# Kernel optimization log

Hardware: AMD Instinct MI355X
Metric: run time of the kernel (lower is better)

## Reference

```python
import jax, jax.numpy as jnp
import numpy as np

H = 16  # n_heads


def setup_inputs() -> dict:
    key = jax.random.key(0)
    ks = jax.random.split(key, 11)
    B, S, D = 2, 2048, 1024
    def rn(k, shape, scale=1.0):
        return jax.random.normal(k, shape, dtype=jnp.float32) * scale
    w_scale = 1.0 / np.sqrt(D)
    return {
        "queries": rn(ks[0], (B, S, D)),
        "keys": rn(ks[1], (B, S, D)),
        "values": rn(ks[2], (B, S, D)),
        "Wq": rn(ks[3], (D, D), w_scale), "bq": rn(ks[4], (D,), 0.02),
        "Wk": rn(ks[5], (D, D), w_scale), "bk": rn(ks[6], (D,), 0.02),
        "Wv": rn(ks[7], (D, D), w_scale), "bv": rn(ks[8], (D,), 0.02),
        "Wo": rn(ks[9], (D, D), w_scale), "bo": rn(ks[10], (D,), 0.02),
    }


def _split_heads(x, h):
    # [B, S, D] -> [B, h, S, D/h]
    B, S, D = x.shape
    return x.reshape(B, S, h, D // h).transpose(0, 2, 1, 3)


def reference(queries, keys, values, Wq, bq, Wk, bk, Wv, bv, Wo, bo):
    B, S, D = queries.shape
    Q = _split_heads(queries @ Wq + bq, H)  # [B,h,S,dk]
    K = _split_heads(keys @ Wk + bk, H)
    V = _split_heads(values @ Wv + bv, H)
    # Faithful quirk: scale by sqrt(seq_len), not sqrt(d_k)
    factor = jnp.sqrt(jnp.asarray(S, dtype=Q.dtype))
    scores = jnp.einsum("bhqd,bhkd->bhqk", Q, K) / factor  # [B,h,S,S]
    weights = jax.nn.softmax(scores, axis=-1)
    attn = jnp.einsum("bhqk,bhkd->bhqd", weights, V)  # [B,h,S,dk]
    attn = attn.transpose(0, 2, 1, 3).reshape(B, S, D)  # [B,S,D]
    return attn @ Wo + bo
```

## Files before the change

kernel.cpp:

```cpp
#include <hip/hip_runtime.h>

typedef unsigned short ushort_t;
typedef unsigned int uint_t;
typedef __attribute__((ext_vector_type(8))) short short8;
typedef __attribute__((ext_vector_type(4))) float floatx4;

#define QSCALE 0.03187936f

__device__ __forceinline__ ushort_t f2bf(float f) {
    union { float f; uint_t u; } c; c.f = f;
    uint_t u = c.u;
    return (ushort_t)((u + 0x7fffu + ((u >> 16) & 1u)) >> 16);
}
__device__ __forceinline__ floatx4 mfma16x32(short8 a, short8 b, floatx4 c) {
    return __builtin_amdgcn_mfma_f32_16x16x32_bf16(a, b, c, 0, 0, 0);
}
__device__ __forceinline__ floatx4 zero4() { floatx4 z = {0.f, 0.f, 0.f, 0.f}; return z; }

__device__ __forceinline__ void gload16(const ushort_t* g, ushort_t* l) {
    __builtin_amdgcn_global_load_lds(
        (const __attribute__((address_space(1))) void*)g,
        (__attribute__((address_space(3))) void*)l, 16, 0, 0);
}

__global__ __launch_bounds__(256) void cvt_bf16(
    const float* __restrict__ s0, const float* __restrict__ s1,
    const float* __restrict__ s2, ushort_t* __restrict__ d0,
    ushort_t* __restrict__ d1, ushort_t* __restrict__ d2)
{
    const int which = blockIdx.x >> 11;
    const int blk = blockIdx.x & 2047;
    const float* src = (which == 0) ? s0 : (which == 1) ? s1 : s2;
    ushort_t* dst = (which == 0) ? d0 : (which == 1) ? d1 : d2;
    const int i = (blk * 256 + threadIdx.x) * 8;
    float4 f0 = *(const float4*)(src + i);
    float4 f1 = *(const float4*)(src + i + 4);
    __align__(16) ushort_t t[8];
    t[0] = f2bf(f0.x); t[1] = f2bf(f0.y); t[2] = f2bf(f0.z); t[3] = f2bf(f0.w);
    t[4] = f2bf(f1.x); t[5] = f2bf(f1.y); t[6] = f2bf(f1.z); t[7] = f2bf(f1.w);
    *(uint4*)(dst + i) = *(uint4*)t;
}

__global__ __launch_bounds__(256) void transpose_w(
    const float* __restrict__ W0, const float* __restrict__ W1,
    const float* __restrict__ W2, const float* __restrict__ W3,
    ushort_t* __restrict__ WT)
{
    __shared__ ushort_t tile[64][65];
    const float* W = (blockIdx.y == 0) ? W0 : (blockIdx.y == 1) ? W1
                   : (blockIdx.y == 2) ? W2 : W3;
    ushort_t* dst = WT + (size_t)blockIdx.y * (1024 * 1024);
    const int t = threadIdx.x;
    const int r = t >> 2, p = t & 3;
    const int j0 = (blockIdx.x & 15) << 6, k0 = (blockIdx.x >> 4) << 6;

    const float* src = W + (size_t)(k0 + r) * 1024 + j0 + p * 16;
    float4 f0 = *(const float4*)(src);
    float4 f1 = *(const float4*)(src + 4);
    float4 f2 = *(const float4*)(src + 8);
    float4 f3 = *(const float4*)(src + 12);
    ushort_t* tr = &tile[r][p * 16];
    tr[0] = f2bf(f0.x); tr[1] = f2bf(f0.y); tr[2]  = f2bf(f0.z); tr[3]  = f2bf(f0.w);
    tr[4] = f2bf(f1.x); tr[5] = f2bf(f1.y); tr[6]  = f2bf(f1.z); tr[7]  = f2bf(f1.w);
    tr[8] = f2bf(f2.x); tr[9] = f2bf(f2.y); tr[10] = f2bf(f2.z); tr[11] = f2bf(f2.w);
    tr[12] = f2bf(f3.x); tr[13] = f2bf(f3.y); tr[14] = f2bf(f3.z); tr[15] = f2bf(f3.w);
    __syncthreads();
    __align__(16) ushort_t buf[16];
#pragma unroll
    for (int i = 0; i < 16; ++i) buf[i] = tile[p * 16 + i][r];
    ushort_t* o = dst + (size_t)(j0 + r) * 1024 + k0 + p * 16;
    *(uint4*)(o)     = *(uint4*)(buf);
    *(uint4*)(o + 8) = *(uint4*)(buf + 8);
}

__global__ __launch_bounds__(256) void gemm_bt(
    const ushort_t* __restrict__ A0, const ushort_t* __restrict__ A1,
    const ushort_t* __restrict__ A2, const ushort_t* __restrict__ WT,
    const float* __restrict__ b0, const float* __restrict__ b1,
    const float* __restrict__ b2,
    ushort_t* __restrict__ Dq, ushort_t* __restrict__ Dk,
    ushort_t* __restrict__ Dv, int zbase)
{
    __shared__ __align__(16) ushort_t As[128 * 32];
    __shared__ __align__(16) ushort_t Bs[128 * 32];

    const int mode = blockIdx.z + zbase;
    const ushort_t* A = (mode == 0) ? A0 : (mode == 1) ? A1 : A2;
    const float* bias = (mode == 0) ? b0 : (mode == 1) ? b1 : b2;
    const ushort_t* Bt = WT + (size_t)mode * 1048576;

    const int tid = threadIdx.x;
    const int lane = tid & 63, wid = tid >> 6;
    const int quad = lane >> 4, l16 = lane & 15;
    const int wm = wid >> 1, wn = wid & 1;
    const int row0 = blockIdx.y << 7, col0 = blockIdx.x << 7;

    floatx4 acc[4][4];
#pragma unroll
    for (int i = 0; i < 4; ++i)
#pragma unroll
        for (int j = 0; j < 4; ++j) acc[i][j] = zero4();

    const int i0 = tid, i1 = 256 + tid;
    const int r0_ = i0 >> 2, c0_ = (i0 & 3) ^ (r0_ & 3);
    const int r1_ = i1 >> 2, c1_ = (i1 & 3) ^ (r1_ & 3);
    const ushort_t* gA0 = A  + (size_t)(row0 + r0_) * 1024 + c0_ * 8;
    const ushort_t* gA1 = A  + (size_t)(row0 + r1_) * 1024 + c1_ * 8;
    const ushort_t* gB0 = Bt + (size_t)(col0 + r0_) * 1024 + c0_ * 8;
    const ushort_t* gB1 = Bt + (size_t)(col0 + r1_) * 1024 + c1_ * 8;
    ushort_t* lA0 = As + i0 * 8;  ushort_t* lA1 = As + i1 * 8;
    ushort_t* lB0 = Bs + i0 * 8;  ushort_t* lB1 = Bs + i1 * 8;

    const int ra = wm * 64 + l16, rb = wn * 64 + l16;
    const int sa_off = (quad ^ (l16 & 3)) * 8;

    for (int k0 = 0; k0 < 1024; k0 += 32) {
        __syncthreads();
        gload16(gA0 + k0, lA0);
        gload16(gA1 + k0, lA1);
        gload16(gB0 + k0, lB0);
        gload16(gB1 + k0, lB1);
        __syncthreads();

        short8 af[4], bf[4];
#pragma unroll
        for (int i = 0; i < 4; ++i)
            af[i] = *(const short8*)(As + (ra + i * 16) * 32 + sa_off);
#pragma unroll
        for (int j = 0; j < 4; ++j)
            bf[j] = *(const short8*)(Bs + (rb + j * 16) * 32 + sa_off);
#pragma unroll
        for (int i = 0; i < 4; ++i)
#pragma unroll
            for (int j = 0; j < 4; ++j)
                acc[i][j] = mfma16x32(af[i], bf[j], acc[i][j]);
    }

    const float sc = (mode == 0) ? QSCALE : 1.f;
#pragma unroll
    for (int i = 0; i < 4; ++i) {
#pragma unroll
        for (int j = 0; j < 4; ++j) {
            const int c = col0 + wn * 64 + j * 16 + l16;
            const float bv = bias[c];
#pragma unroll
            for (int rr = 0; rr < 4; ++rr) {
                const int r = row0 + wm * 64 + i * 16 + quad * 4 + rr;
                const float v = (acc[i][j][rr] + bv) * sc;
                const int b = r >> 11, s = r & 2047, h = c >> 6, d = c & 63;
                if (mode <= 1) {
                    ushort_t* D = (mode == 0) ? Dq : Dk;
                    D[(((b * 16 + h) * 2048 + s) << 6) + d] = f2bf(v);
                } else {
                    Dv[(((b * 16 + h) * 64 + d) << 11) + s] = f2bf(v);
                }
            }
        }
    }
}

__global__ __launch_bounds__(256) void gemm64(
    const ushort_t* __restrict__ A, const ushort_t* __restrict__ Bt,
    const float* __restrict__ bias, float* __restrict__ Dout)
{
    __shared__ __align__(16) ushort_t As[64 * 32];
    __shared__ __align__(16) ushort_t Bs[128 * 32];
    const int tid = threadIdx.x;
    const int lane = tid & 63, wid = tid >> 6;
    const int quad = lane >> 4, l16 = lane & 15;
    const int wm = wid >> 1, wn = wid & 1;
    const int row0 = blockIdx.y << 6, col0 = blockIdx.x << 7;

    floatx4 acc[2][4];
#pragma unroll
    for (int i = 0; i < 2; ++i)
#pragma unroll
        for (int j = 0; j < 4; ++j) acc[i][j] = zero4();

    const int rA = tid >> 2, cA = (tid & 3) ^ (rA & 3);
    const ushort_t* gA = A + (size_t)(row0 + rA) * 1024 + cA * 8;
    ushort_t* lA = As + tid * 8;
    const int i0 = tid, i1 = 256 + tid;
    const int rB0 = i0 >> 2, cB0 = (i0 & 3) ^ (rB0 & 3);
    const int rB1 = i1 >> 2, cB1 = (i1 & 3) ^ (rB1 & 3);
    const ushort_t* gB0 = Bt + (size_t)(col0 + rB0) * 1024 + cB0 * 8;
    const ushort_t* gB1 = Bt + (size_t)(col0 + rB1) * 1024 + cB1 * 8;
    ushort_t* lB0 = Bs + i0 * 8;  ushort_t* lB1 = Bs + i1 * 8;

    const int sa_off = (quad ^ (l16 & 3)) * 8;

    for (int k0 = 0; k0 < 1024; k0 += 32) {
        __syncthreads();
        gload16(gA + k0, lA);
        gload16(gB0 + k0, lB0);
        gload16(gB1 + k0, lB1);
        __syncthreads();

        short8 af[2], bf[4];
#pragma unroll
        for (int i = 0; i < 2; ++i)
            af[i] = *(const short8*)(As + (wm * 32 + i * 16 + l16) * 32 + sa_off);
#pragma unroll
        for (int j = 0; j < 4; ++j)
            bf[j] = *(const short8*)(Bs + (wn * 64 + j * 16 + l16) * 32 + sa_off);
#pragma unroll
        for (int i = 0; i < 2; ++i)
#pragma unroll
            for (int j = 0; j < 4; ++j)
                acc[i][j] = mfma16x32(af[i], bf[j], acc[i][j]);
    }

#pragma unroll
    for (int i = 0; i < 2; ++i)
#pragma unroll
        for (int j = 0; j < 4; ++j) {
            const int c = col0 + wn * 64 + j * 16 + l16;
            const float bv = bias[c];
#pragma unroll
            for (int rr = 0; rr < 4; ++rr) {
                const int r = row0 + wm * 32 + i * 16 + quad * 4 + rr;
                Dout[(size_t)r * 1024 + c] = acc[i][j][rr] + bv;
            }
        }
}

__global__ __launch_bounds__(256, 2) void attn64q(
    const ushort_t* __restrict__ Q, const ushort_t* __restrict__ K,
    const ushort_t* __restrict__ Vt, ushort_t* __restrict__ Out)
{
    __shared__ __align__(16) ushort_t Ks[2][2][64 * 64];
    __shared__ __align__(16) ushort_t Vs[2][2][64 * 64];

    const int tid = threadIdx.x;
    const int lane = tid & 63, wid = tid >> 6;
    const int quad = lane >> 4, l16 = lane & 15;
    const int blk = blockIdx.x;
    const int bh = blk & 31;
    const int q0 = (blk >> 5) << 7;

    const ushort_t* Qh = Q + (size_t)bh * (2048 * 64);
    const ushort_t* Kh = K + (size_t)bh * (2048 * 64);
    const ushort_t* Vh = Vt + (size_t)bh * (64 * 2048);

    short8 qf0[2], qf1[2];
#pragma unroll
    for (int u = 0; u < 2; ++u) {
        const int qr = q0 + wid * 32 + u * 16 + l16;
        qf0[u] = *(const short8*)(Qh + (size_t)qr * 64 + quad * 8);
        qf1[u] = *(const short8*)(Qh + (size_t)qr * 64 + 32 + quad * 8);
    }

    floatx4 o_acc[2][4], lsum[2];
#pragma unroll
    for (int u = 0; u < 2; ++u) {
        lsum[u] = zero4();
#pragma unroll
        for (int d = 0; d < 4; ++d) o_acc[u][d] = zero4();
    }

    const int kr = tid >> 3, kc = (tid & 7) ^ (kr & 7);
    const ushort_t* gK0 = Kh + (size_t)kr * 64 + kc * 8;
    const ushort_t* gV0 = Vh + (size_t)kr * 2048 + kc * 8;

    const int l7 = l16 & 7;
    const int q2 = quad >> 1, q1 = (quad & 1) * 4;

    union { uint_t u4[4]; short8 s; } onep;
    onep.u4[0] = onep.u4[1] = onep.u4[2] = onep.u4[3] = 0x3f803f80u;
    const short8 ones = onep.s;

#define STAGE(pp, kto) do {                                                  \
        _Pragma("unroll")                                                    \
        for (int hf_ = 0; hf_ < 2; ++hf_) {                                  \
            gload16(gK0 + (size_t)(kto) * 64 + hf_ * 4096,                   \
                    &Ks[pp][hf_][tid * 8]);                                  \
            gload16(gK0 + (size_t)(kto) * 64 + hf_ * 4096 + 2048,            \
                    &Ks[pp][hf_][tid * 8 + 2048]);                           \
            gload16(gV0 + (kto) + hf_ * 64,                                  \
                    &Vs[pp][hf_][tid * 8]);                                  \
            gload16(gV0 + (kto) + hf_ * 64 + 65536,                          \
                    &Vs[pp][hf_][tid * 8 + 2048]);                           \
        }                                                                    \
    } while (0)

    STAGE(0, 0);
    for (int it = 0; it < 16; ++it) {
        const int p = it & 1;
        __syncthreads();
        if (it < 15) STAGE(p ^ 1, (it + 1) * 128);

#pragma unroll
        for (int hf = 0; hf < 2; ++hf) {
            const ushort_t* ksp = &Ks[p][hf][0];
            const ushort_t* vsp = &Vs[p][hf][0];

            floatx4 sa[2][4];
#pragma unroll
            for (int g = 0; g < 4; ++g) {
                const int row = g * 16 + l16;
                const short8 kf0 = *(const short8*)(ksp + row * 64 + ((quad ^ l7) * 8));
                const short8 kf1 = *(const short8*)(ksp + row * 64 + (((quad + 4) ^ l7) * 8));
#pragma unroll
                for (int u = 0; u < 2; ++u) {
                    floatx4 t0 = mfma16x32(kf0, qf0[u], zero4());
                    sa[u][g] = mfma16x32(kf1, qf1[u], t0);
                }
            }

#pragma unroll
            for (int G = 0; G < 2; ++G) {
                short8 pf[2];
#pragma unroll
                for (int u = 0; u < 2; ++u) {
                    uint_t ub[8];
#pragma unroll
                    for (int t = 0; t < 8; ++t) {
                        const int g = G * 2 + (t >> 2), r = t & 3;
                        const float e = __builtin_amdgcn_exp2f(fminf(sa[u][g][r], 80.f));
                        ub[t] = __float_as_uint(e);
                    }
                    union { uint_t u4[4]; short8 s; } pc;
                    pc.u4[0] = __builtin_amdgcn_perm(ub[1], ub[0], 0x07060302u);
                    pc.u4[1] = __builtin_amdgcn_perm(ub[3], ub[2], 0x07060302u);
                    pc.u4[2] = __builtin_amdgcn_perm(ub[5], ub[4], 0x07060302u);
                    pc.u4[3] = __builtin_amdgcn_perm(ub[7], ub[6], 0x07060302u);
                    pf[u] = pc.s;
                    lsum[u] = mfma16x32(pf[u], ones, lsum[u]);
                }
                const int ch0 = ((4 * G + q2) ^ l7) * 8;
                const int ch1 = ((4 * G + 2 + q2) ^ l7) * 8;
#pragma unroll
                for (int db = 0; db < 4; ++db) {
                    const int vbase = (db * 16 + l16) * 64 + q1;
                    const uint2 v0 = *(const uint2*)(vsp + vbase + ch0);
                    const uint2 v1 = *(const uint2*)(vsp + vbase + ch1);
                    union { uint_t u4[4]; short8 s; } vc;
                    vc.u4[0] = v0.x; vc.u4[1] = v0.y; vc.u4[2] = v1.x; vc.u4[3] = v1.y;
                    o_acc[0][db] = mfma16x32(pf[0], vc.s, o_acc[0][db]);
                    o_acc[1][db] = mfma16x32(pf[1], vc.s, o_acc[1][db]);
                }
            }
        }
    }
#undef STAGE

    const int b = bh >> 4, hh = bh & 15;
#pragma unroll
    for (int u = 0; u < 2; ++u) {
        const int s0 = q0 + wid * 32 + u * 16 + quad * 4;
#pragma unroll
        for (int r = 0; r < 4; ++r) {
            const float inv = 1.f / lsum[u][r];
#pragma unroll
            for (int db = 0; db < 4; ++db) {
                const float v = o_acc[u][db][r] * inv;
                Out[(size_t)(b * 2048 + s0 + r) * 1024 + hh * 64 + db * 16 + l16] = f2bf(v);
            }
        }
    }
}

extern "C" void kernel_launch(void* const* d_in, const int* in_sizes, int n_in,
                              void* d_out, int out_size, void* d_ws, size_t ws_size,
                              hipStream_t stream) {
    const float* queries = (const float*)d_in[0];
    const float* keys    = (const float*)d_in[1];
    const float* values  = (const float*)d_in[2];
    const float* Wq = (const float*)d_in[3];
    const float* bq = (const float*)d_in[4];
    const float* Wk = (const float*)d_in[5];
    const float* bk = (const float*)d_in[6];
    const float* Wv = (const float*)d_in[7];
    const float* bv = (const float*)d_in[8];
    const float* Wo = (const float*)d_in[9];
    const float* bo = (const float*)d_in[10];
    float* out = (float*)d_out;

    char* ws = (char*)d_ws;
    const size_t MB = 1024 * 1024;
    ushort_t* WT = (ushort_t*)(ws);
    const ushort_t* WoT = WT + 3 * 1048576;
    dim3 tb(256);

    transpose_w<<<dim3(256, 4), tb, 0, stream>>>(Wq, Wk, Wv, Wo, WT);

    if (ws_size >= 64 * MB) {
        ushort_t* Qb  = (ushort_t*)(ws + 8 * MB);
        ushort_t* Kb  = (ushort_t*)(ws + 16 * MB);
        ushort_t* Vb  = (ushort_t*)(ws + 24 * MB);
        ushort_t* Qp  = (ushort_t*)(ws + 32 * MB);
        ushort_t* Kp  = (ushort_t*)(ws + 40 * MB);
        ushort_t* Vtp = (ushort_t*)(ws + 48 * MB);
        ushort_t* An  = (ushort_t*)(ws + 56 * MB);
        cvt_bf16<<<dim3(6144), tb, 0, stream>>>(queries, keys, values, Qb, Kb, Vb);
        gemm_bt<<<dim3(8, 32, 3), tb, 0, stream>>>(Qb, Kb, Vb, WT,
            bq, bk, bv, Qp, Kp, Vtp, 0);
        attn64q<<<dim3(512), tb, 0, stream>>>(Qp, Kp, Vtp, An);
        gemm64<<<dim3(8, 64), tb, 0, stream>>>(An, WoT, bo, out);
    } else {
        ushort_t* buf1 = (ushort_t*)(ws + 8 * MB);
        ushort_t* buf2 = (ushort_t*)(ws + 16 * MB);
        ushort_t* Qp   = (ushort_t*)(ws + 24 * MB);
        ushort_t* Kp   = (ushort_t*)(ws + 32 * MB);
        cvt_bf16<<<dim3(4096), tb, 0, stream>>>(queries, keys, keys, buf1, buf2, buf2);
        gemm_bt<<<dim3(8, 32, 2), tb, 0, stream>>>(buf1, buf2, buf2, WT,
            bq, bk, bk, Qp, Kp, Kp, 0);
        cvt_bf16<<<dim3(2048), tb, 0, stream>>>(values, values, values, buf1, buf1, buf1);
        gemm_bt<<<dim3(8, 32, 1), tb, 0, stream>>>(buf1, buf1, buf1, WT,
            bv, bv, bv, buf2, buf2, buf2, 2);
        attn64q<<<dim3(512), tb, 0, stream>>>(Qp, Kp, buf2, buf1);
        gemm64<<<dim3(8, 64), tb, 0, stream>>>(buf1, WoT, bo, out);
    }
}
```

Baseline: 229.6 us.

## Split attention block across 8 waves with 16 query rows each

The attention kernel now launches 512 threads per block, so each of the eight waves owns 16 query rows instead of 32. Each thread issues half as many K/V tile loads into LDS, and per-thread accumulator and score register use is halved. The goal is more waves in flight to hide latency and better balance the MFMA and exp work. In exchange each K/V fragment read from LDS feeds only one MFMA instead of two, which doubles LDS read traffic per unit of compute, and the larger blocks may limit how many fit on a CU.

```diff
diff --git a/kernel.cpp b/kernel.cpp
--- a/kernel.cpp
+++ b/kernel.cpp
@@ -224,7 +224,7 @@
         }
 }
 
-__global__ __launch_bounds__(256, 2) void attn64q(
+__global__ __launch_bounds__(512, 2) void attn64q(
     const ushort_t* __restrict__ Q, const ushort_t* __restrict__ K,
     const ushort_t* __restrict__ Vt, ushort_t* __restrict__ Out)
 {
@@ -242,21 +242,13 @@
     const ushort_t* Kh = K + (size_t)bh * (2048 * 64);
     const ushort_t* Vh = Vt + (size_t)bh * (64 * 2048);
 
-    short8 qf0[2], qf1[2];
-#pragma unroll
-    for (int u = 0; u < 2; ++u) {
-        const int qr = q0 + wid * 32 + u * 16 + l16;
-        qf0[u] = *(const short8*)(Qh + (size_t)qr * 64 + quad * 8);
-        qf1[u] = *(const short8*)(Qh + (size_t)qr * 64 + 32 + quad * 8);
-    }
-
-    floatx4 o_acc[2][4], lsum[2];
-#pragma unroll
-    for (int u = 0; u < 2; ++u) {
-        lsum[u] = zero4();
-#pragma unroll
-        for (int d = 0; d < 4; ++d) o_acc[u][d] = zero4();
-    }
+    const int qr = q0 + wid * 16 + l16;
+    const short8 qf0 = *(const short8*)(Qh + (size_t)qr * 64 + quad * 8);
+    const short8 qf1 = *(const short8*)(Qh + (size_t)qr * 64 + 32 + quad * 8);
+
+    floatx4 o_acc[4], lsum = zero4();
+#pragma unroll
+    for (int d = 0; d < 4; ++d) o_acc[d] = zero4();
 
     const int kr = tid >> 3, kc = (tid & 7) ^ (kr & 7);
     const ushort_t* gK0 = Kh + (size_t)kr * 64 + kc * 8;
@@ -274,12 +266,8 @@
         for (int hf_ = 0; hf_ < 2; ++hf_) {                                  \
             gload16(gK0 + (size_t)(kto) * 64 + hf_ * 4096,                   \
                     &Ks[pp][hf_][tid * 8]);                                  \
-            gload16(gK0 + (size_t)(kto) * 64 + hf_ * 4096 + 2048,            \
-                    &Ks[pp][hf_][tid * 8 + 2048]);                           \
             gload16(gV0 + (kto) + hf_ * 64,                                  \
                     &Vs[pp][hf_][tid * 8]);                                  \
-            gload16(gV0 + (kto) + hf_ * 64 + 65536,                          \
-                    &Vs[pp][hf_][tid * 8 + 2048]);                           \
         }                                                                    \
     } while (0)
 
@@ -294,39 +282,33 @@
             const ushort_t* ksp = &Ks[p][hf][0];
             const ushort_t* vsp = &Vs[p][hf][0];
 
-            floatx4 sa[2][4];
+            floatx4 sa[4];
 #pragma unroll
             for (int g = 0; g < 4; ++g) {
                 const int row = g * 16 + l16;
                 const short8 kf0 = *(const short8*)(ksp + row * 64 + ((quad ^ l7) * 8));
                 const short8 kf1 = *(const short8*)(ksp + row * 64 + (((quad + 4) ^ l7) * 8));
-#pragma unroll
-                for (int u = 0; u < 2; ++u) {
-                    floatx4 t0 = mfma16x32(kf0, qf0[u], zero4());
-                    sa[u][g] = mfma16x32(kf1, qf1[u], t0);
+                floatx4 t0 = mfma16x32(kf0, qf0, zero4());
+                sa[g] = mfma16x32(kf1, qf1, t0);
+            }
+
+#pragma unroll
+            for (int G = 0; G < 2; ++G) {
+                uint_t ub[8];
+#pragma unroll
+                for (int t = 0; t < 8; ++t) {
+                    const int g = G * 2 + (t >> 2), r = t & 3;
+                    const float e = __builtin_amdgcn_exp2f(fminf(sa[g][r], 80.f));
+                    ub[t] = __float_as_uint(e);
                 }
-            }
-
-#pragma unroll
-            for (int G = 0; G < 2; ++G) {
-                short8 pf[2];
-#pragma unroll
-                for (int u = 0; u < 2; ++u) {
-                    uint_t ub[8];
-#pragma unroll
-                    for (int t = 0; t < 8; ++t) {
-                        const int g = G * 2 + (t >> 2), r = t & 3;
-                        const float e = __builtin_amdgcn_exp2f(fminf(sa[u][g][r], 80.f));
-                        ub[t] = __float_as_uint(e);
-                    }
-                    union { uint_t u4[4]; short8 s; } pc;
-                    pc.u4[0] = __builtin_amdgcn_perm(ub[1], ub[0], 0x07060302u);
-                    pc.u4[1] = __builtin_amdgcn_perm(ub[3], ub[2], 0x07060302u);
-                    pc.u4[2] = __builtin_amdgcn_perm(ub[5], ub[4], 0x07060302u);
-                    pc.u4[3] = __builtin_amdgcn_perm(ub[7], ub[6], 0x07060302u);
-                    pf[u] = pc.s;
-                    lsum[u] = mfma16x32(pf[u], ones, lsum[u]);
-                }
+                union { uint_t u4[4]; short8 s; } pc;
+                pc.u4[0] = __builtin_amdgcn_perm(ub[1], ub[0], 0x07060302u);
+                pc.u4[1] = __builtin_amdgcn_perm(ub[3], ub[2], 0x07060302u);
+                pc.u4[2] = __builtin_amdgcn_perm(ub[5], ub[4], 0x07060302u);
+                pc.u4[3] = __builtin_amdgcn_perm(ub[7], ub[6], 0x07060302u);
+                const short8 pf = pc.s;
+                lsum = mfma16x32(pf, ones, lsum);
+
                 const int ch0 = ((4 * G + q2) ^ l7) * 8;
                 const int ch1 = ((4 * G + 2 + q2) ^ l7) * 8;
 #pragma unroll
@@ -336,8 +318,7 @@
                     const uint2 v1 = *(const uint2*)(vsp + vbase + ch1);
                     union { uint_t u4[4]; short8 s; } vc;
                     vc.u4[0] = v0.x; vc.u4[1] = v0.y; vc.u4[2] = v1.x; vc.u4[3] = v1.y;
-                    o_acc[0][db] = mfma16x32(pf[0], vc.s, o_acc[0][db]);
-                    o_acc[1][db] = mfma16x32(pf[1], vc.s, o_acc[1][db]);
+                    o_acc[db] = mfma16x32(pf, vc.s, o_acc[db]);
                 }
             }
         }
@@ -345,17 +326,14 @@
 #undef STAGE
 
     const int b = bh >> 4, hh = bh & 15;
-#pragma unroll
-    for (int u = 0; u < 2; ++u) {
-        const int s0 = q0 + wid * 32 + u * 16 + quad * 4;
-#pragma unroll
-        for (int r = 0; r < 4; ++r) {
-            const float inv = 1.f / lsum[u][r];
-#pragma unroll
-            for (int db = 0; db < 4; ++db) {
-                const float v = o_acc[u][db][r] * inv;
-                Out[(size_t)(b * 2048 + s0 + r) * 1024 + hh * 64 + db * 16 + l16] = f2bf(v);
-            }
+    const int s0 = q0 + wid * 16 + quad * 4;
+#pragma unroll
+    for (int r = 0; r < 4; ++r) {
+        const float inv = 1.f / lsum[r];
+#pragma unroll
+        for (int db = 0; db < 4; ++db) {
+            const float v = o_acc[db][r] * inv;
+            Out[(size_t)(b * 2048 + s0 + r) * 1024 + hh * 64 + db * 16 + l16] = f2bf(v);
         }
     }
 }
@@ -381,6 +359,7 @@
     ushort_t* WT = (ushort_t*)(ws);
     const ushort_t* WoT = WT + 3 * 1048576;
     dim3 tb(256);
+    dim3 ta(512);
 
     transpose_w<<<dim3(256, 4), tb, 0, stream>>>(Wq, Wk, Wv, Wo, WT);
 
@@ -395,7 +374,7 @@
         cvt_bf16<<<dim3(6144), tb, 0, stream>>>(queries, keys, values, Qb, Kb, Vb);
         gemm_bt<<<dim3(8, 32, 3), tb, 0, stream>>>(Qb, Kb, Vb, WT,
             bq, bk, bv, Qp, Kp, Vtp, 0);
-        attn64q<<<dim3(512), tb, 0, stream>>>(Qp, Kp, Vtp, An);
+        attn64q<<<dim3(512), ta, 0, stream>>>(Qp, Kp, Vtp, An);
         gemm64<<<dim3(8, 64), tb, 0, stream>>>(An, WoT, bo, out);
     } else {
         ushort_t* buf1 = (ushort_t*)(ws + 8 * MB);
@@ -408,7 +387,7 @@
         cvt_bf16<<<dim3(2048), tb, 0, stream>>>(values, values, values, buf1, buf1, buf1);
         gemm_bt<<<dim3(8, 32, 1), tb, 0, stream>>>(buf1, buf1, buf1, WT,
             bv, bv, bv, buf2, buf2, buf2, 2);
-        attn64q<<<dim3(512), tb, 0, stream>>>(Qp, Kp, buf2, buf1);
+        attn64q<<<dim3(512), ta, 0, stream>>>(Qp, Kp, buf2, buf1);
         gemm64<<<dim3(8, 64), tb, 0, stream>>>(buf1, WoT, bo, out);
     }
 }
```

Result: no change. 228.9 us (-0.3%).

## Fuse weight transpose into input conversion and remap GEMM blocks across XCDs

Applied to the files above, without the earlier changes.

Merges the bf16 conversion of inputs and the weight transpose/convert into one `prep` kernel, removing a separate launch. Both GEMM kernels now use a flat 1-D grid with a swizzled block index, so consecutive tiles sharing A/B panels land on the same XCD and its L2 cache. The transposed V projection epilogue now writes four consecutive sequence elements as one 8-byte store instead of four scalar stores. Costs are extra index arithmetic, and the fallback path now converts `keys` twice inside `prep`.

```diff
diff --git a/kernel.cpp b/kernel.cpp
--- a/kernel.cpp
+++ b/kernel.cpp
@@ -21,6 +21,59 @@
     __builtin_amdgcn_global_load_lds(
         (const __attribute__((address_space(1))) void*)g,
         (__attribute__((address_space(3))) void*)l, 16, 0, 0);
+}
+
+__global__ __launch_bounds__(256) void prep(
+    const float* __restrict__ s0, const float* __restrict__ s1,
+    const float* __restrict__ s2, ushort_t* __restrict__ d0,
+    ushort_t* __restrict__ d1, ushort_t* __restrict__ d2,
+    const float* __restrict__ W0, const float* __restrict__ W1,
+    const float* __restrict__ W2, const float* __restrict__ W3,
+    ushort_t* __restrict__ WT)
+{
+    __shared__ ushort_t tile[64][65];
+    const int bid = blockIdx.x;
+    if (bid < 6144) {
+        const int which = bid >> 11;
+        const int blk = bid & 2047;
+        const float* src = (which == 0) ? s0 : (which == 1) ? s1 : s2;
+        ushort_t* dst = (which == 0) ? d0 : (which == 1) ? d1 : d2;
+        const int i = (blk * 256 + threadIdx.x) * 8;
+        float4 f0 = *(const float4*)(src + i);
+        float4 f1 = *(const float4*)(src + i + 4);
+        __align__(16) ushort_t t[8];
+        t[0] = f2bf(f0.x); t[1] = f2bf(f0.y); t[2] = f2bf(f0.z); t[3] = f2bf(f0.w);
+        t[4] = f2bf(f1.x); t[5] = f2bf(f1.y); t[6] = f2bf(f1.z); t[7] = f2bf(f1.w);
+        *(uint4*)(dst + i) = *(uint4*)t;
+        return;
+    }
+    const int tb_ = bid - 6144;
+    const int wsel = tb_ >> 8;
+    const int bx = tb_ & 255;
+    const float* W = (wsel == 0) ? W0 : (wsel == 1) ? W1
+                   : (wsel == 2) ? W2 : W3;
+    ushort_t* dst = WT + (size_t)wsel * (1024 * 1024);
+    const int t = threadIdx.x;
+    const int r = t >> 2, p = t & 3;
+    const int j0 = (bx & 15) << 6, k0 = (bx >> 4) << 6;
+
+    const float* src = W + (size_t)(k0 + r) * 1024 + j0 + p * 16;
+    float4 f0 = *(const float4*)(src);
+    float4 f1 = *(const float4*)(src + 4);
+    float4 f2 = *(const float4*)(src + 8);
+    float4 f3 = *(const float4*)(src + 12);
+    ushort_t* tr = &tile[r][p * 16];
+    tr[0] = f2bf(f0.x); tr[1] = f2bf(f0.y); tr[2]  = f2bf(f0.z); tr[3]  = f2bf(f0.w);
+    tr[4] = f2bf(f1.x); tr[5] = f2bf(f1.y); tr[6]  = f2bf(f1.z); tr[7]  = f2bf(f1.w);
+    tr[8] = f2bf(f2.x); tr[9] = f2bf(f2.y); tr[10] = f2bf(f2.z); tr[11] = f2bf(f2.w);
+    tr[12] = f2bf(f3.x); tr[13] = f2bf(f3.y); tr[14] = f2bf(f3.z); tr[15] = f2bf(f3.w);
+    __syncthreads();
+    __align__(16) ushort_t buf[16];
+#pragma unroll
+    for (int i = 0; i < 16; ++i) buf[i] = tile[p * 16 + i][r];
+    ushort_t* o = dst + (size_t)(j0 + r) * 1024 + k0 + p * 16;
+    *(uint4*)(o)     = *(uint4*)(buf);
+    *(uint4*)(o + 8) = *(uint4*)(buf + 8);
 }
 
 __global__ __launch_bounds__(256) void cvt_bf16(
@@ -41,38 +94,6 @@
     *(uint4*)(dst + i) = *(uint4*)t;
 }
 
-__global__ __launch_bounds__(256) void transpose_w(
-    const float* __restrict__ W0, const float* __restrict__ W1,
-    const float* __restrict__ W2, const float* __restrict__ W3,
-    ushort_t* __restrict__ WT)
-{
-    __shared__ ushort_t tile[64][65];
-    const float* W = (blockIdx.y == 0) ? W0 : (blockIdx.y == 1) ? W1
-                   : (blockIdx.y == 2) ? W2 : W3;
-    ushort_t* dst = WT + (size_t)blockIdx.y * (1024 * 1024);
-    const int t = threadIdx.x;
-    const int r = t >> 2, p = t & 3;
-    const int j0 = (blockIdx.x & 15) << 6, k0 = (blockIdx.x >> 4) << 6;
-
-    const float* src = W + (size_t)(k0 + r) * 1024 + j0 + p * 16;
-    float4 f0 = *(const float4*)(src);
-    float4 f1 = *(const float4*)(src + 4);
-    float4 f2 = *(const float4*)(src + 8);
-    float4 f3 = *(const float4*)(src + 12);
-    ushort_t* tr = &tile[r][p * 16];
-    tr[0] = f2bf(f0.x); tr[1] = f2bf(f0.y); tr[2]  = f2bf(f0.z); tr[3]  = f2bf(f0.w);
-    tr[4] = f2bf(f1.x); tr[5] = f2bf(f1.y); tr[6]  = f2bf(f1.z); tr[7]  = f2bf(f1.w);
-    tr[8] = f2bf(f2.x); tr[9] = f2bf(f2.y); tr[10] = f2bf(f2.z); tr[11] = f2bf(f2.w);
-    tr[12] = f2bf(f3.x); tr[13] = f2bf(f3.y); tr[14] = f2bf(f3.z); tr[15] = f2bf(f3.w);
-    __syncthreads();
-    __align__(16) ushort_t buf[16];
-#pragma unroll
-    for (int i = 0; i < 16; ++i) buf[i] = tile[p * 16 + i][r];
-    ushort_t* o = dst + (size_t)(j0 + r) * 1024 + k0 + p * 16;
-    *(uint4*)(o)     = *(uint4*)(buf);
-    *(uint4*)(o + 8) = *(uint4*)(buf + 8);
-}
-
 __global__ __launch_bounds__(256) void gemm_bt(
     const ushort_t* __restrict__ A0, const ushort_t* __restrict__ A1,
     const ushort_t* __restrict__ A2, const ushort_t* __restrict__ WT,
@@ -84,7 +105,12 @@
     __shared__ __align__(16) ushort_t As[128 * 32];
     __shared__ __align__(16) ushort_t Bs[128 * 32];
 
-    const int mode = blockIdx.z + zbase;
+    const int bid = blockIdx.x;
+    const int cpx = gridDim.x >> 3;
+    const int vbid = (bid & 7) * cpx + (bid >> 3);
+    const int bx = vbid & 7, by = (vbid >> 3) & 31, bz = vbid >> 8;
+
+    const int mode = bz + zbase;
     const ushort_t* A = (mode == 0) ? A0 : (mode == 1) ? A1 : A2;
     const float* bias = (mode == 0) ? b0 : (mode == 1) ? b1 : b2;
     const ushort_t* Bt = WT + (size_t)mode * 1048576;
@@ -93,7 +119,7 @@
     const int lane = tid & 63, wid = tid >> 6;
     const int quad = lane >> 4, l16 = lane & 15;
     const int wm = wid >> 1, wn = wid & 1;
-    const int row0 = blockIdx.y << 7, col0 = blockIdx.x << 7;
+    const int row0 = by << 7, col0 = bx << 7;
 
     floatx4 acc[4][4];
 #pragma unroll
@@ -143,17 +169,23 @@
         for (int j = 0; j < 4; ++j) {
             const int c = col0 + wn * 64 + j * 16 + l16;
             const float bv = bias[c];
-#pragma unroll
-            for (int rr = 0; rr < 4; ++rr) {
-                const int r = row0 + wm * 64 + i * 16 + quad * 4 + rr;
-                const float v = (acc[i][j][rr] + bv) * sc;
-                const int b = r >> 11, s = r & 2047, h = c >> 6, d = c & 63;
-                if (mode <= 1) {
-                    ushort_t* D = (mode == 0) ? Dq : Dk;
-                    D[(((b * 16 + h) * 2048 + s) << 6) + d] = f2bf(v);
-                } else {
-                    Dv[(((b * 16 + h) * 64 + d) << 11) + s] = f2bf(v);
+            const int rbase = row0 + wm * 64 + i * 16 + quad * 4;
+            const int b = rbase >> 11, s0 = rbase & 2047;
+            const int h = c >> 6, d = c & 63;
+            if (mode <= 1) {
+                ushort_t* D = (mode == 0) ? Dq : Dk;
+#pragma unroll
+                for (int rr = 0; rr < 4; ++rr) {
+                    const float v = (acc[i][j][rr] + bv) * sc;
+                    D[(((b * 16 + h) * 2048 + s0 + rr) << 6) + d] = f2bf(v);
                 }
+            } else {
+                __align__(8) ushort_t t4[4];
+#pragma unroll
+                for (int rr = 0; rr < 4; ++rr)
+                    t4[rr] = f2bf(acc[i][j][rr] + bv);
+                *(uint2*)(Dv + (((size_t)(b * 16 + h) * 64 + d) << 11) + s0) =
+                    *(const uint2*)t4;
             }
         }
     }
@@ -165,11 +197,16 @@
 {
     __shared__ __align__(16) ushort_t As[64 * 32];
     __shared__ __align__(16) ushort_t Bs[128 * 32];
+    const int bid = blockIdx.x;
+    const int cpx = gridDim.x >> 3;
+    const int vbid = (bid & 7) * cpx + (bid >> 3);
+    const int bx = vbid & 7, by = vbid >> 3;
+
     const int tid = threadIdx.x;
     const int lane = tid & 63, wid = tid >> 6;
     const int quad = lane >> 4, l16 = lane & 15;
     const int wm = wid >> 1, wn = wid & 1;
-    const int row0 = blockIdx.y << 6, col0 = blockIdx.x << 7;
+    const int row0 = by << 6, col0 = bx << 7;
 
     floatx4 acc[2][4];
 #pragma unroll
@@ -382,8 +419,6 @@
     const ushort_t* WoT = WT + 3 * 1048576;
     dim3 tb(256);
 
-    transpose_w<<<dim3(256, 4), tb, 0, stream>>>(Wq, Wk, Wv, Wo, WT);
-
     if (ws_size >= 64 * MB) {
         ushort_t* Qb  = (ushort_t*)(ws + 8 * MB);
         ushort_t* Kb  = (ushort_t*)(ws + 16 * MB);
@@ -392,23 +427,25 @@
         ushort_t* Kp  = (ushort_t*)(ws + 40 * MB);
         ushort_t* Vtp = (ushort_t*)(ws + 48 * MB);
         ushort_t* An  = (ushort_t*)(ws + 56 * MB);
-        cvt_bf16<<<dim3(6144), tb, 0, stream>>>(queries, keys, values, Qb, Kb, Vb);
-        gemm_bt<<<dim3(8, 32, 3), tb, 0, stream>>>(Qb, Kb, Vb, WT,
+        prep<<<dim3(7168), tb, 0, stream>>>(queries, keys, values, Qb, Kb, Vb,
+            Wq, Wk, Wv, Wo, WT);
+        gemm_bt<<<dim3(768), tb, 0, stream>>>(Qb, Kb, Vb, WT,
             bq, bk, bv, Qp, Kp, Vtp, 0);
         attn64q<<<dim3(512), tb, 0, stream>>>(Qp, Kp, Vtp, An);
-        gemm64<<<dim3(8, 64), tb, 0, stream>>>(An, WoT, bo, out);
+        gemm64<<<dim3(512), tb, 0, stream>>>(An, WoT, bo, out);
     } else {
         ushort_t* buf1 = (ushort_t*)(ws + 8 * MB);
         ushort_t* buf2 = (ushort_t*)(ws + 16 * MB);
         ushort_t* Qp   = (ushort_t*)(ws + 24 * MB);
         ushort_t* Kp   = (ushort_t*)(ws + 32 * MB);
-        cvt_bf16<<<dim3(4096), tb, 0, stream>>>(queries, keys, keys, buf1, buf2, buf2);
-        gemm_bt<<<dim3(8, 32, 2), tb, 0, stream>>>(buf1, buf2, buf2, WT,
+        prep<<<dim3(7168), tb, 0, stream>>>(queries, keys, keys, buf1, buf2, buf2,
+            Wq, Wk, Wv, Wo, WT);
+        gemm_bt<<<dim3(512), tb, 0, stream>>>(buf1, buf2, buf2, WT,
             bq, bk, bk, Qp, Kp, Kp, 0);
         cvt_bf16<<<dim3(2048), tb, 0, stream>>>(values, values, values, buf1, buf1, buf1);
-        gemm_bt<<<dim3(8, 32, 1), tb, 0, stream>>>(buf1, buf1, buf1, WT,
+        gemm_bt<<<dim3(256), tb, 0, stream>>>(buf1, buf1, buf1, WT,
             bv, bv, bv, buf2, buf2, buf2, 2);
         attn64q<<<dim3(512), tb, 0, stream>>>(Qp, Kp, buf2, buf1);
-        gemm64<<<dim3(8, 64), tb, 0, stream>>>(buf1, WoT, bo, out);
-    }
-}
+        gemm64<<<dim3(512), tb, 0, stream>>>(buf1, WoT, bo, out);
+    }
+}
```

Measured after the change: 230.5 us. No clear change (+0.4%).
